# Kernel tuning notes

Hardware: AMD Instinct MI355X
Metric: run time of the kernel (lower is better)

The kernel has to match this reference:

```python
import jax, jax.numpy as jnp
import numpy as np

H = W_DIM = 4096
K = 7
STRIDE = 2

def setup_inputs() -> dict:
    key = jax.random.key(0)
    k1, k2 = jax.random.split(key)
    X = jax.random.normal(k1, (H, W_DIM), dtype=jnp.float32)
    W = jax.random.normal(k2, (K, K), dtype=jnp.float32)
    return {"X": X, "W": W}

def reference(X, W):
    # Strided valid cross-correlation of a single 2D image with a single 2D filter.
    # Equivalent to the nested-loop torch.sum(torch.mul(W, X[i:i+K, j:j+K])).
    lhs = X[None, None, :, :]          # NCHW: (1,1,H,W)
    rhs = W[None, None, :, :]          # OIHW: (1,1,K,K)
    out = jax.lax.conv_general_dilated(
        lhs, rhs,
        window_strides=(STRIDE, STRIDE),
        padding='VALID',
        dimension_numbers=('NCHW', 'OIHW', 'NCHW'),
    )
    return out[0, 0]                   # (floor((H-K+S)/S), floor((W-K+S)/S)) = (2045, 2045)
```

## Files before the change

### kernel.cpp

```cpp
#include <hip/hip_runtime.h>
#include <stdint.h>


static constexpr int H     = 4096;
static constexpr int OUT   = 2045;
static constexpr int P4    = 36;
static constexpr int ROWS  = 69;
static constexpr int SLOTS = ROWS * P4;
static constexpr int NIT   = (SLOTS + 255) / 256;
static constexpr int NT    = 4;

__global__ __launch_bounds__(256) void conv7s2_kernel(
    const float* __restrict__ X,
    const float* __restrict__ W,
    float* __restrict__ out)
{
    __shared__ float4 lds4[2][SLOTS];

    const int t = threadIdx.x;
    const int b = blockIdx.x;

    float w[49];
#pragma unroll
    for (int i = 0; i < 49; ++i) w[i] = W[i];

    int lrowA[NIT], chA[NIT];
#pragma unroll
    for (int it = 0; it < NIT; ++it) {
        const int l  = t + 256 * it;
        const int lr = l / P4;
        const int u  = l - lr * P4;
        lrowA[it] = lr;
        chA[it]   = u ^ ((lr >> 2) & 3);
    }

    const int tysub = t & 3;
    const int c     = (t >> 2) & 15;
    const int wv    = t >> 6;
    const int rg    = tysub + 4 * wv;
    const int c2    = 2 * c;

    auto stage = [&](int buf, int tid) {
        const int C0 = (tid & 31) * 128;
        const int R0 = (tid >> 5) * 64;
#pragma unroll
        for (int it = 0; it < NIT; ++it) {
            const int l = t + 256 * it;
            if (l < SLOTS) {
                int grow = R0 + lrowA[it];     if (grow > H - 1) grow = H - 1;
                int gcol = C0 + 4 * chA[it];   if (gcol > H - 4) gcol = H - 4;
                const float* gp = X + (size_t)grow * H + gcol;
                __builtin_amdgcn_global_load_lds(
                    (const __attribute__((address_space(1))) uint32_t*)gp,
                    (__attribute__((address_space(3))) uint32_t*)&lds4[buf][l],
                    16, 0, 0);
            }
        }
    };

    stage(0, 4 * b);
    __syncthreads();

#pragma unroll
    for (int k = 0; k < NT; ++k) {
        const int cur = k & 1;
        const int tid = 4 * b + k;
        const int bx  = tid & 31;
        const int by  = tid >> 5;

        if (k + 1 < NT) stage(cur ^ 1, tid + 1);

        float acc0[4] = {0.f, 0.f, 0.f, 0.f};
        float acc1[4] = {0.f, 0.f, 0.f, 0.f};

#pragma unroll
        for (int r = 0; r < 9; ++r) {
            const int lrow = 4 * rg + r;
            const int base = lrow * P4;
            const int s    = (rg + (r >> 2)) & 3;

            float rv[16];
#pragma unroll
            for (int i = 0; i < 4; ++i) {
                const float4 v = lds4[cur][base + ((c2 + i) ^ s)];
                rv[4 * i + 0] = v.x;
                rv[4 * i + 1] = v.y;
                rv[4 * i + 2] = v.z;
                rv[4 * i + 3] = v.w;
            }

#pragma unroll
            for (int q = 0; q < 7; ++q) {
#pragma unroll
                for (int j = 0; j < 4; ++j) {
                    const float cv = rv[2 * j + q];
                    if (r <= 6) acc0[j] = fmaf(cv, w[r * 7 + q],       acc0[j]);
                    if (r >= 2) acc1[j] = fmaf(cv, w[(r - 2) * 7 + q], acc1[j]);
                }
            }
        }

        const int x0 = bx * 64 + 4 * c;
        const int y0 = by * 32 + 2 * rg;
#pragma unroll
        for (int j = 0; j < 4; ++j) {
            const int x = x0 + j;
            if (x < OUT) {
                if (y0     < OUT) out[(size_t)y0       * OUT + x] = acc0[j];
                if (y0 + 1 < OUT) out[(size_t)(y0 + 1) * OUT + x] = acc1[j];
            }
        }

        if (k + 1 < NT) __syncthreads();
    }
}

extern "C" void kernel_launch(void* const* d_in, const int* in_sizes, int n_in,
                              void* d_out, int out_size, void* d_ws, size_t ws_size,
                              hipStream_t stream) {
    const float* X = (const float*)d_in[0];
    const float* W = (const float*)d_in[1];
    float* out = (float*)d_out;

    conv7s2_kernel<<<dim3(512), 256, 0, stream>>>(X, W, out);
}
```

Before: 23.71 us.

## Overlap next-tile LDS staging with compute via partial vmcnt waits and new swizzle

Removes the per-load bounds predicate by padding the LDS buffers to a full multiple of 256 slots. It replaces __syncthreads with explicit s_waitcnt vmcnt(10) plus raw s_barrier, so the prefetch of the next tile stays in flight while the current tile is consumed. The XOR swizzle changes to a different bit pattern that leaves the last columns unswizzled, aiming to reduce LDS bank conflicts. The hard-coded vmcnt relies on the compiler emitting exactly 10 loads per stage in order; if it does not, the wait may be wrong and the result incorrect.

```diff
diff --git a/kernel.cpp b/kernel.cpp
--- a/kernel.cpp
+++ b/kernel.cpp
@@ -7,15 +7,23 @@
 static constexpr int P4    = 36;
 static constexpr int ROWS  = 69;
 static constexpr int SLOTS = ROWS * P4;
-static constexpr int NIT   = (SLOTS + 255) / 256;
+static constexpr int NIT   = 10;
+static constexpr int ALLOC = NIT * 256;
 static constexpr int NT    = 4;
+
+__device__ __forceinline__ int sel(int q) {
+    return (q & 1) | ((q & 2) << 1);
+}
+__device__ __forceinline__ int swz(int u, int s) {
+    return (u < 32) ? (u ^ s) : u;
+}
 
 __global__ __launch_bounds__(256) void conv7s2_kernel(
     const float* __restrict__ X,
     const float* __restrict__ W,
     float* __restrict__ out)
 {
-    __shared__ float4 lds4[2][SLOTS];
+    __shared__ float4 lds4[2][ALLOC];
 
     const int t = threadIdx.x;
     const int b = blockIdx.x;
@@ -24,14 +32,14 @@
 #pragma unroll
     for (int i = 0; i < 49; ++i) w[i] = W[i];
 
-    int lrowA[NIT], chA[NIT];
+    int lrowA[NIT], G4A[NIT];
 #pragma unroll
     for (int it = 0; it < NIT; ++it) {
         const int l  = t + 256 * it;
         const int lr = l / P4;
         const int u  = l - lr * P4;
         lrowA[it] = lr;
-        chA[it]   = u ^ ((lr >> 2) & 3);
+        G4A[it]   = 4 * swz(u, sel((lr >> 2) & 3));
     }
 
     const int tysub = t & 3;
@@ -46,29 +54,32 @@
 #pragma unroll
         for (int it = 0; it < NIT; ++it) {
             const int l = t + 256 * it;
-            if (l < SLOTS) {
-                int grow = R0 + lrowA[it];     if (grow > H - 1) grow = H - 1;
-                int gcol = C0 + 4 * chA[it];   if (gcol > H - 4) gcol = H - 4;
-                const float* gp = X + (size_t)grow * H + gcol;
-                __builtin_amdgcn_global_load_lds(
-                    (const __attribute__((address_space(1))) uint32_t*)gp,
-                    (__attribute__((address_space(3))) uint32_t*)&lds4[buf][l],
-                    16, 0, 0);
-            }
+            int grow = R0 + lrowA[it];  if (grow > H - 1) grow = H - 1;
+            int gcol = C0 + G4A[it];    if (gcol > H - 4) gcol = H - 4;
+            const float* gp = X + (size_t)grow * H + gcol;
+            __builtin_amdgcn_global_load_lds(
+                (const __attribute__((address_space(1))) uint32_t*)gp,
+                (__attribute__((address_space(3))) uint32_t*)&lds4[buf][l],
+                16, 0, 0);
         }
     };
 
     stage(0, 4 * b);
-    __syncthreads();
 
 #pragma unroll
     for (int k = 0; k < NT; ++k) {
-        const int cur = k & 1;
         const int tid = 4 * b + k;
         const int bx  = tid & 31;
         const int by  = tid >> 5;
+        const int cur = k & 1;
 
         if (k + 1 < NT) stage(cur ^ 1, tid + 1);
+
+        if (k + 1 < NT) { asm volatile("s_waitcnt vmcnt(10)" ::: "memory"); }
+        else           { asm volatile("s_waitcnt vmcnt(0)"  ::: "memory"); }
+        __builtin_amdgcn_sched_barrier(0);
+        __builtin_amdgcn_s_barrier();
+        __builtin_amdgcn_sched_barrier(0);
 
         float acc0[4] = {0.f, 0.f, 0.f, 0.f};
         float acc1[4] = {0.f, 0.f, 0.f, 0.f};
@@ -77,12 +88,12 @@
         for (int r = 0; r < 9; ++r) {
             const int lrow = 4 * rg + r;
             const int base = lrow * P4;
-            const int s    = (rg + (r >> 2)) & 3;
+            const int s    = sel((rg + (r >> 2)) & 3);
 
             float rv[16];
 #pragma unroll
             for (int i = 0; i < 4; ++i) {
-                const float4 v = lds4[cur][base + ((c2 + i) ^ s)];
+                const float4 v = lds4[cur][base + swz(c2 + i, s)];
                 rv[4 * i + 0] = v.x;
                 rv[4 * i + 1] = v.y;
                 rv[4 * i + 2] = v.z;
@@ -111,7 +122,11 @@
             }
         }
 
-        if (k + 1 < NT) __syncthreads();
+        if (k + 1 < NT) {
+            __builtin_amdgcn_sched_barrier(0);
+            __builtin_amdgcn_s_barrier();
+            __builtin_amdgcn_sched_barrier(0);
+        }
     }
 }
 
```

Result: slower. 24.28 us (+2.4%).
